# Optimization experiments

Measured on AMD Instinct MI355X. Metric: run time of the kernel, lower is better.

## Reference

```python
import jax, jax.numpy as jnp
import numpy as np

B, C, H, W = 16, 128, 48, 48
C4 = C // 4
N = H * W
BN_EPS = 1e-5


def conv_bn_relu(x, w, gamma, beta, mean, var):
    # 1x1 conv (no bias) as channel contraction, then eval-mode BatchNorm, then ReLU
    y = jnp.einsum('bchw,oc->bohw', x, w)
    scale = gamma / jnp.sqrt(var + BN_EPS)
    y = y * scale[None, :, None, None] + (beta - mean * scale)[None, :, None, None]
    return jax.nn.relu(y)


def setup_inputs() -> dict:
    key = jax.random.key(0)
    ks = jax.random.split(key, 16)
    inp = {
        'x_en': jax.random.normal(ks[0], (B, C, H, W), dtype=jnp.float32),
        'x_de': jax.random.normal(ks[1], (B, C, H, W), dtype=jnp.float32),
        'x_cat': jax.random.normal(ks[2], (B, 2 * C, H, W), dtype=jnp.float32),
        # Get_KQ: Conv2d(C -> C/4, 1x1, no bias) + BN(C/4) (shared for K and Q)
        'w_kq': jax.random.normal(ks[3], (C4, C), dtype=jnp.float32) * 0.05,
        'kq_gamma': jax.random.normal(ks[4], (C4,), dtype=jnp.float32) * 0.1 + 1.0,
        'kq_beta': jax.random.normal(ks[5], (C4,), dtype=jnp.float32) * 0.1,
        'kq_mean': jax.random.normal(ks[6], (C4,), dtype=jnp.float32) * 0.1,
        'kq_var': jax.random.uniform(ks[7], (C4,), dtype=jnp.float32) + 0.5,
        # Get_V: Conv2d(C -> C, 1x1, no bias) + BN(C)
        'w_v': jax.random.normal(ks[8], (C, C), dtype=jnp.float32) * 0.05,
        'v_gamma': jax.random.normal(ks[9], (C,), dtype=jnp.float32) * 0.1 + 1.0,
        'v_beta': jax.random.normal(ks[10], (C,), dtype=jnp.float32) * 0.1,
        'v_mean': jax.random.normal(ks[11], (C,), dtype=jnp.float32) * 0.1,
        'v_var': jax.random.uniform(ks[12], (C,), dtype=jnp.float32) + 0.5,
        # reduce_channels: Conv2d(2C -> C, 1x1, no bias) + BN(C)
        'w_red': jax.random.normal(ks[13], (C, 2 * C), dtype=jnp.float32) * 0.05,
        'red_gamma': jax.random.normal(ks[14], (C,), dtype=jnp.float32) * 0.1 + 1.0,
        'red_beta': jax.random.normal(ks[15], (C,), dtype=jnp.float32) * 0.1,
        'red_mean': jax.random.normal(jax.random.fold_in(key, 100), (C,), dtype=jnp.float32) * 0.1,
        'red_var': jax.random.uniform(jax.random.fold_in(key, 101), (C,), dtype=jnp.float32) + 0.5,
    }
    return inp


def reference(x_en, x_de, x_cat,
              w_kq, kq_gamma, kq_beta, kq_mean, kq_var,
              w_v, v_gamma, v_beta, v_mean, v_var,
              w_red, red_gamma, red_beta, red_mean, red_var):
    Kf = conv_bn_relu(x_en, w_kq, kq_gamma, kq_beta, kq_mean, kq_var).reshape(B, C4, N)
    Qf = conv_bn_relu(x_de, w_kq, kq_gamma, kq_beta, kq_mean, kq_var).reshape(B, C4, N)
    # KQ[b, n, m] = sum_k K[b, k, n] * Q[b, k, m]  -> [B, N, N]
    KQ = jnp.einsum('bkn,bkm->bnm', Kf, Qf)
    # GLOBAL softmax over the flattened N*N map (per batch), not per row
    A = jax.nn.softmax(KQ.reshape(B, N * N), axis=1).reshape(B, N, N)
    x = conv_bn_relu(x_cat, w_red, red_gamma, red_beta, red_mean, red_var)
    V = conv_bn_relu(x, w_v, v_gamma, v_beta, v_mean, v_var).reshape(B, C, N)
    # FeatureMap[b, c, n] = sum_m V[b, c, m] * A[b, n, m]
    feat = jnp.einsum('bcm,bnm->bcn', V, A).reshape(B, C, H, W)
    return jnp.concatenate([x, feat], axis=1)
```

## Files before the change

kernel.cpp:

```cpp
#include <hip/hip_runtime.h>
#include <math.h>

#define C    128
#define C4   32
#define NN   2304
#define BN_EPS 1e-5f
#define NEG_INF -3.402823466e38f
#define LOG2E 1.4426950408889634f

typedef short bf16x8 __attribute__((ext_vector_type(8)));
typedef float f32x4 __attribute__((ext_vector_type(4)));

#define SOFT_BARRIER() asm volatile("s_waitcnt lgkmcnt(0)\n\ts_barrier" ::: "memory")

__device__ inline unsigned short f2bf(float f) {
    unsigned int u = __float_as_uint(f);
    u += 0x7fffu + ((u >> 16) & 1u);
    return (unsigned short)(u >> 16);
}

__device__ inline unsigned int pk2bf(float a, float b) {
#if __has_builtin(__builtin_amdgcn_cvt_pk_bf16_f32)
    typedef __bf16 bf2 __attribute__((ext_vector_type(2)));
    bf2 v = __builtin_amdgcn_cvt_pk_bf16_f32(a, b);
    return __builtin_bit_cast(unsigned int, v);
#else
    unsigned int ua = __float_as_uint(a); ua += 0x7fffu + ((ua >> 16) & 1u);
    unsigned int ub = __float_as_uint(b); ub += 0x7fffu + ((ub >> 16) & 1u);
    return __builtin_amdgcn_perm(ub, ua, 0x07060302u);
#endif
}

__device__ inline float fexp2(float x) {
#if __has_builtin(__builtin_amdgcn_exp2f)
    return __builtin_amdgcn_exp2f(x);
#else
    return __expf(x * 0.69314718055994531f);
#endif
}


__global__ __launch_bounds__(256) void k_wprep(
    const float* __restrict__ wkq, const float* __restrict__ kq_g,
    const float* __restrict__ kq_b, const float* __restrict__ kq_m,
    const float* __restrict__ kq_v,
    const float* __restrict__ wv, const float* __restrict__ v_g,
    const float* __restrict__ v_b, const float* __restrict__ v_m,
    const float* __restrict__ v_v,
    const float* __restrict__ wred, const float* __restrict__ red_g,
    const float* __restrict__ red_b, const float* __restrict__ red_m,
    const float* __restrict__ red_v,
    unsigned short* __restrict__ wkq_bf, unsigned short* __restrict__ wv_bf,
    unsigned short* __restrict__ wred_bf,
    float* __restrict__ kq_sh, float* __restrict__ v_sh, float* __restrict__ red_sh)
{
    const int t = blockIdx.x * 256 + threadIdx.x;
    if (t < 4096) {
        const int o = t >> 7;
        const float sc = kq_g[o] * rsqrtf(kq_v[o] + BN_EPS);
        wkq_bf[t] = f2bf(wkq[t] * sc);
        if ((t & 127) == 0) kq_sh[o] = kq_b[o] - kq_m[o] * sc;
    } else if (t < 4096 + 16384) {
        const int e = t - 4096;
        const int o = e >> 7;
        const float sc = v_g[o] * rsqrtf(v_v[o] + BN_EPS);
        wv_bf[e] = f2bf(wv[e] * sc);
        if ((e & 127) == 0) v_sh[o] = v_b[o] - v_m[o] * sc;
    } else if (t < 4096 + 16384 + 32768) {
        const int e = t - 20480;
        const int o = e >> 8;
        const float sc = red_g[o] * rsqrtf(red_v[o] + BN_EPS);
        wred_bf[e] = f2bf(wred[e] * sc);
        if ((e & 255) == 0) red_sh[o] = red_b[o] - red_m[o] * sc;
    }
}

__global__ __launch_bounds__(256) void k_kq(
    const float* __restrict__ x0, const float* __restrict__ x1,
    const unsigned short* __restrict__ wbf, const float* __restrict__ shift,
    unsigned short* __restrict__ Kt, unsigned short* __restrict__ Qt)
{
    constexpr int NTILE = 128, R = 8;
    __shared__ unsigned short Xs[2][NTILE][40];

    const int tid = threadIdx.x;
    const int w = tid >> 6, lane = tid & 63;
    const int quad = lane >> 4, l16 = lane & 15;
    const int b = blockIdx.y, n0 = blockIdx.x * NTILE;
    const int nbase = w * 32;

    const float* xin = (blockIdx.z ? x1 : x0) + (size_t)b * C * NN;
    const int p = tid & 15, g = tid >> 4;

    f32x4 acc[2][2];
#pragma unroll
    for (int mt = 0; mt < 2; mt++)
#pragma unroll
        for (int nt = 0; nt < 2; nt++) acc[mt][nt] = (f32x4){0.f, 0.f, 0.f, 0.f};

    const float* xrb = xin + n0 + g * R;
    float av[R], bv[R];
    {
        const float* xr = xrb + (size_t)(2 * p) * NN;
#pragma unroll
        for (int i4 = 0; i4 < R; i4 += 4) {
            *(float4*)&av[i4] = *(const float4*)&xr[i4];
            *(float4*)&bv[i4] = *(const float4*)&xr[NN + i4];
        }
    }

    for (int k = 0; k < 4; ++k) {
        unsigned int uu[R];
#pragma unroll
        for (int i = 0; i < R; i++) uu[i] = pk2bf(av[i], bv[i]);
        if (k < 3) {
            const float* xr = xrb + (size_t)((k + 1) * 32 + 2 * p) * NN;
#pragma unroll
            for (int i4 = 0; i4 < R; i4 += 4) {
                *(float4*)&av[i4] = *(const float4*)&xr[i4];
                *(float4*)&bv[i4] = *(const float4*)&xr[NN + i4];
            }
        }
        unsigned int* Xw = (unsigned int*)Xs[k & 1];
#pragma unroll
        for (int i = 0; i < R; i++)
            Xw[(g * R + i) * 20 + p] = uu[i];
        SOFT_BARRIER();
        bf16x8 af[2];
#pragma unroll
        for (int mt = 0; mt < 2; mt++)
            af[mt] = *(const bf16x8*)&wbf[(size_t)(mt * 16 + l16) * C + k * 32 + quad * 8];
#pragma unroll
        for (int nt = 0; nt < 2; nt++) {
            const bf16x8 bfr = *(const bf16x8*)&Xs[k & 1][nbase + nt * 16 + l16][quad * 8];
#pragma unroll
            for (int mt = 0; mt < 2; mt++)
                acc[mt][nt] = __builtin_amdgcn_mfma_f32_16x16x32_bf16(af[mt], bfr, acc[mt][nt], 0, 0, 0);
        }
    }

    unsigned short* ob16 = blockIdx.z ? Qt : Kt;
    const float osc = blockIdx.z ? 1.f : LOG2E;
#pragma unroll
    for (int mt = 0; mt < 2; mt++)
#pragma unroll
        for (int nt = 0; nt < 2; nt++)
#pragma unroll
            for (int r = 0; r < 4; r++) {
                const int o = mt * 16 + quad * 4 + r;
                const int n = n0 + nbase + nt * 16 + l16;
                const float sh = shift[o];
                ob16[((size_t)b * NN + n) * 32 + o] =
                    f2bf(fmaxf(acc[mt][nt][r] + sh, 0.f) * osc);
            }
}

__global__ __launch_bounds__(256) void k_redv(
    const float* __restrict__ xcat,
    const unsigned short* __restrict__ wred_bf, const float* __restrict__ red_sh,
    const unsigned short* __restrict__ wv_bf,  const float* __restrict__ v_sh,
    float* __restrict__ out, unsigned short* __restrict__ Vf)
{
    __shared__ unsigned short Xs[2][48][40];
    __shared__ unsigned int   Xv[64 * 49];

    const int tid = threadIdx.x;
    const int w = tid >> 6, lane = tid & 63;
    const int quad = lane >> 4, l16 = lane & 15;
    const int b = blockIdx.y, n0 = blockIdx.x * 48;
    const float* xin = xcat + (size_t)b * 2 * C * NN;
    const int p = tid & 15, g = tid >> 4;

    f32x4 acc[2][3];
#pragma unroll
    for (int mt = 0; mt < 2; mt++)
#pragma unroll
        for (int nt = 0; nt < 3; nt++) acc[mt][nt] = (f32x4){0.f, 0.f, 0.f, 0.f};

    float4 av, bv;
    if (g < 12) {
        const float* xr = xin + (size_t)(2 * p) * NN + n0 + g * 4;
        av = *(const float4*)&xr[0];
        bv = *(const float4*)&xr[NN];
    }

    for (int k = 0; k < 8; ++k) {
        if (g < 12) {
            const unsigned int u0 = pk2bf(av.x, bv.x);
            const unsigned int u1 = pk2bf(av.y, bv.y);
            const unsigned int u2 = pk2bf(av.z, bv.z);
            const unsigned int u3 = pk2bf(av.w, bv.w);
            if (k < 7) {
                const float* xr = xin + (size_t)((k + 1) * 32 + 2 * p) * NN + n0 + g * 4;
                av = *(const float4*)&xr[0];
                bv = *(const float4*)&xr[NN];
            }
            unsigned int* Xw = (unsigned int*)Xs[k & 1];
            Xw[(g * 4 + 0) * 20 + p] = u0;
            Xw[(g * 4 + 1) * 20 + p] = u1;
            Xw[(g * 4 + 2) * 20 + p] = u2;
            Xw[(g * 4 + 3) * 20 + p] = u3;
        }
        SOFT_BARRIER();
        bf16x8 af[2];
#pragma unroll
        for (int mt = 0; mt < 2; mt++)
            af[mt] = *(const bf16x8*)&wred_bf[(size_t)(w * 32 + mt * 16 + l16) * (2 * C) + k * 32 + quad * 8];
#pragma unroll
        for (int nt = 0; nt < 3; nt++) {
            const bf16x8 bfr = *(const bf16x8*)&Xs[k & 1][nt * 16 + l16][quad * 8];
#pragma unroll
            for (int mt = 0; mt < 2; mt++)
                acc[mt][nt] = __builtin_amdgcn_mfma_f32_16x16x32_bf16(af[mt], bfr, acc[mt][nt], 0, 0, 0);
        }
    }

    {
        float* ob = out + (size_t)b * (2 * C * NN);
#pragma unroll
        for (int mt = 0; mt < 2; mt++) {
            float sh[4];
#pragma unroll
            for (int r = 0; r < 4; r++) sh[r] = red_sh[w * 32 + mt * 16 + quad * 4 + r];
#pragma unroll
            for (int nt = 0; nt < 3; nt++) {
                const int n = n0 + nt * 16 + l16;
                float v[4];
#pragma unroll
                for (int r = 0; r < 4; r++) {
                    const int o = w * 32 + mt * 16 + quad * 4 + r;
                    v[r] = fmaxf(acc[mt][nt][r] + sh[r], 0.f);
                    ob[(size_t)o * NN + n] = v[r];
                }
                const int op0 = 16 * w + mt * 8 + quad * 2;
                Xv[(op0 + 0) * 49 + nt * 16 + l16] = pk2bf(v[0], v[1]);
                Xv[(op0 + 1) * 49 + nt * 16 + l16] = pk2bf(v[2], v[3]);
            }
        }
    }
    SOFT_BARRIER();

    f32x4 vacc[2][3];
#pragma unroll
    for (int mt = 0; mt < 2; mt++)
#pragma unroll
        for (int nt = 0; nt < 3; nt++) vacc[mt][nt] = (f32x4){0.f, 0.f, 0.f, 0.f};

    for (int c0 = 0; c0 < C; c0 += 32) {
        bf16x8 af[2];
#pragma unroll
        for (int mt = 0; mt < 2; mt++)
            af[mt] = *(const bf16x8*)&wv_bf[(size_t)(w * 32 + mt * 16 + l16) * C + c0 + quad * 8];
#pragma unroll
        for (int nt = 0; nt < 3; nt++) {
            const int col = nt * 16 + l16;
            const int cp0 = c0 / 2 + quad * 4;
            uint4 u;
            u.x = Xv[(cp0 + 0) * 49 + col];
            u.y = Xv[(cp0 + 1) * 49 + col];
            u.z = Xv[(cp0 + 2) * 49 + col];
            u.w = Xv[(cp0 + 3) * 49 + col];
            const bf16x8 bfr = __builtin_bit_cast(bf16x8, u);
#pragma unroll
            for (int mt = 0; mt < 2; mt++)
                vacc[mt][nt] = __builtin_amdgcn_mfma_f32_16x16x32_bf16(af[mt], bfr, vacc[mt][nt], 0, 0, 0);
        }
    }

#pragma unroll
    for (int mt = 0; mt < 2; mt++) {
        float sh[4];
#pragma unroll
        for (int r = 0; r < 4; r++) sh[r] = v_sh[w * 32 + mt * 16 + quad * 4 + r];
#pragma unroll
        for (int nt = 0; nt < 3; nt++)
#pragma unroll
            for (int r = 0; r < 4; r++) {
                const int o = w * 32 + mt * 16 + quad * 4 + r;
                const int n = n0 + nt * 16 + l16;
                Vf[((size_t)b * C + o) * NN + n] = f2bf(fmaxf(vacc[mt][nt][r] + sh[r], 0.f));
            }
    }
}

__global__ __launch_bounds__(256) void k_stats(
    const unsigned short* __restrict__ Kt, const unsigned short* __restrict__ Qt,
    float* __restrict__ bmax, float* __restrict__ bsum)
{
    const int tid = threadIdx.x;
    const int w = tid >> 6, lane = tid & 63;
    const int quad = lane >> 4, l16 = lane & 15;
    const int wg = blockIdx.x;
    const int xcd = wg & 7;
    const int slot = wg >> 3;
    const int b = xcd * 2 + slot / 324;
    const int tile = slot % 324;
    const int my = tile / 18, mx = tile % 18;
    const int n0 = mx * 128, m0 = my * 128;
    const unsigned short* Kb = Kt + (size_t)b * NN * 32;
    const unsigned short* Qb = Qt + (size_t)b * NN * 32;

    bf16x8 kf[8], qf[2];
#pragma unroll
    for (int nt = 0; nt < 8; nt++)
        kf[nt] = *(const bf16x8*)&Kb[(size_t)(n0 + nt * 16 + l16) * 32 + quad * 8];
#pragma unroll
    for (int mt = 0; mt < 2; mt++)
        qf[mt] = *(const bf16x8*)&Qb[(size_t)(m0 + w * 32 + mt * 16 + l16) * 32 + quad * 8];

    f32x4 s[16];
#pragma unroll
    for (int mt = 0; mt < 2; mt++)
#pragma unroll
        for (int nt = 0; nt < 8; nt++) {
            f32x4 z = (f32x4){0.f, 0.f, 0.f, 0.f};
            s[mt * 8 + nt] = __builtin_amdgcn_mfma_f32_16x16x32_bf16(qf[mt], kf[nt], z, 0, 0, 0);
        }

    float lmax = NEG_INF;
#pragma unroll
    for (int i = 0; i < 16; i++)
        lmax = fmaxf(lmax, fmaxf(fmaxf(s[i][0], s[i][1]), fmaxf(s[i][2], s[i][3])));
    float lsum = 0.f;
#pragma unroll
    for (int i = 0; i < 16; i++)
        lsum += fexp2(s[i][0] - lmax) + fexp2(s[i][1] - lmax) +
                fexp2(s[i][2] - lmax) + fexp2(s[i][3] - lmax);

#pragma unroll
    for (int off = 32; off > 0; off >>= 1) {
        const float omax = __shfl_xor(lmax, off);
        const float osum = __shfl_xor(lsum, off);
        const float nmax = fmaxf(lmax, omax);
        lsum = lsum * fexp2(lmax - nmax) + osum * fexp2(omax - nmax);
        lmax = nmax;
    }
    __shared__ float smax[4], ssum[4];
    if (lane == 0) { smax[w] = lmax; ssum[w] = lsum; }
    __syncthreads();
    if (tid == 0) {
        float M = smax[0], S = ssum[0];
        for (int i = 1; i < 4; i++) {
            const float nmax = fmaxf(M, smax[i]);
            S = S * fexp2(M - nmax) + ssum[i] * fexp2(smax[i] - nmax);
            M = nmax;
        }
        const int idx = (b * 18 + my) * 18 + mx;
        bmax[idx] = M;
        bsum[idx] = S;
    }
}

__global__ __launch_bounds__(256) void k_fin(
    const float* __restrict__ bmax, const float* __restrict__ bsum,
    float* __restrict__ Ms, float* __restrict__ Sinv)
{
    __shared__ float rmax[256], rsum[256];
    const int b = blockIdx.x, tid = threadIdx.x;
    float lmax = NEG_INF, lsum = 0.f;
    for (int i = tid; i < 324; i += 256) {
        const float m = bmax[b * 324 + i], s = bsum[b * 324 + i];
        const float nmax = fmaxf(lmax, m);
        lsum = lsum * fexp2(lmax - nmax) + s * fexp2(m - nmax);
        lmax = nmax;
    }
    rmax[tid] = lmax; rsum[tid] = lsum;
    __syncthreads();
    for (int st = 128; st > 0; st >>= 1) {
        if (tid < st) {
            const float m2 = rmax[tid + st], s2 = rsum[tid + st];
            const float nmax = fmaxf(rmax[tid], m2);
            rsum[tid] = rsum[tid] * fexp2(rmax[tid] - nmax) + s2 * fexp2(m2 - nmax);
            rmax[tid] = nmax;
        }
        __syncthreads();
    }
    if (tid == 0) { Ms[b] = rmax[0]; Sinv[b] = 1.f / rsum[0]; }
}

__global__ __launch_bounds__(256) void k_feat(
    const unsigned short* __restrict__ Kt, const unsigned short* __restrict__ Qt,
    const unsigned short* __restrict__ Vf, const float* __restrict__ Ms,
    const float* __restrict__ Sinv, float* __restrict__ out)
{
    __shared__ __align__(16) unsigned short Et[2][48][136];
    const int tid = threadIdx.x;
    const int w = tid >> 6, lane = tid & 63;
    const int quad = lane >> 4, l16 = lane & 15;
    const int wg = blockIdx.x;
    const int xcd = wg & 7;
    const int slot = wg >> 3;
    const int b = xcd * 2 + slot / 48;
    const int n0 = (slot % 48) * 48;
    const unsigned short* Kb = Kt + (size_t)b * NN * 32;
    const unsigned short* Qb = Qt + (size_t)b * NN * 32;
    const unsigned short* Vb = Vf + (size_t)b * C * NN;
    const float M = Ms[b], Si = Sinv[b];

    bf16x8 kf[3];
#pragma unroll
    for (int nt = 0; nt < 3; nt++)
        kf[nt] = *(const bf16x8*)&Kb[(size_t)(n0 + nt * 16 + l16) * 32 + quad * 8];

    f32x4 acc[2][3];
#pragma unroll
    for (int i = 0; i < 2; i++)
#pragma unroll
        for (int j = 0; j < 3; j++) acc[i][j] = (f32x4){0.f, 0.f, 0.f, 0.f};

    {
        const bf16x8 q00 = *(const bf16x8*)&Qb[(size_t)(w * 32 + l16) * 32 + quad * 8];
        const bf16x8 q01 = *(const bf16x8*)&Qb[(size_t)(w * 32 + 16 + l16) * 32 + quad * 8];
        f32x4 s0[3], s1[3];
#pragma unroll
        for (int nt = 0; nt < 3; nt++) {
            f32x4 z = (f32x4){0.f, 0.f, 0.f, 0.f};
            s0[nt] = __builtin_amdgcn_mfma_f32_16x16x32_bf16(q00, kf[nt], z, 0, 0, 0);
            s1[nt] = __builtin_amdgcn_mfma_f32_16x16x32_bf16(q01, kf[nt], z, 0, 0, 0);
        }
#pragma unroll
        for (int nt = 0; nt < 3; nt++) {
            const unsigned int a0 = pk2bf(fexp2(s0[nt][0] - M), fexp2(s0[nt][1] - M));
            const unsigned int a1 = pk2bf(fexp2(s0[nt][2] - M), fexp2(s0[nt][3] - M));
            *(uint2*)&Et[0][nt * 16 + l16][w * 32 + quad * 4] = make_uint2(a0, a1);
            const unsigned int b0 = pk2bf(fexp2(s1[nt][0] - M), fexp2(s1[nt][1] - M));
            const unsigned int b1 = pk2bf(fexp2(s1[nt][2] - M), fexp2(s1[nt][3] - M));
            *(uint2*)&Et[0][nt * 16 + l16][w * 32 + 16 + quad * 4] = make_uint2(b0, b1);
        }
    }
    bf16x8 qc0 = *(const bf16x8*)&Qb[(size_t)(128 + w * 32 + l16) * 32 + quad * 8];
    bf16x8 qc1 = *(const bf16x8*)&Qb[(size_t)(128 + w * 32 + 16 + l16) * 32 + quad * 8];
    SOFT_BARRIER();

    for (int k = 0; k < 18; ++k) {
        const int cur = k & 1;
        const int m0 = k * 128;
        const int mq = (k + 2 < 18 ? k + 2 : 0) * 128;
        bf16x8 qn0 = *(const bf16x8*)&Qb[(size_t)(mq + w * 32 + l16) * 32 + quad * 8];
        bf16x8 qn1 = *(const bf16x8*)&Qb[(size_t)(mq + w * 32 + 16 + l16) * 32 + quad * 8];
        bf16x8 vc[2][4];
#pragma unroll
        for (int ct = 0; ct < 2; ct++)
#pragma unroll
            for (int ks = 0; ks < 4; ks++)
                vc[ct][ks] = *(const bf16x8*)&Vb[(size_t)(w * 32 + ct * 16 + l16) * NN + m0 + ks * 32 + quad * 8];

        if (k < 17) {
            f32x4 s0[3], s1[3];
#pragma unroll
            for (int nt = 0; nt < 3; nt++) {
                f32x4 z = (f32x4){0.f, 0.f, 0.f, 0.f};
                s0[nt] = __builtin_amdgcn_mfma_f32_16x16x32_bf16(qc0, kf[nt], z, 0, 0, 0);
                s1[nt] = __builtin_amdgcn_mfma_f32_16x16x32_bf16(qc1, kf[nt], z, 0, 0, 0);
            }
#pragma unroll
            for (int nt = 0; nt < 3; nt++) {
                const unsigned int a0 = pk2bf(fexp2(s0[nt][0] - M), fexp2(s0[nt][1] - M));
                const unsigned int a1 = pk2bf(fexp2(s0[nt][2] - M), fexp2(s0[nt][3] - M));
                *(uint2*)&Et[cur ^ 1][nt * 16 + l16][w * 32 + quad * 4] = make_uint2(a0, a1);
                const unsigned int b0 = pk2bf(fexp2(s1[nt][0] - M), fexp2(s1[nt][1] - M));
                const unsigned int b1 = pk2bf(fexp2(s1[nt][2] - M), fexp2(s1[nt][3] - M));
                *(uint2*)&Et[cur ^ 1][nt * 16 + l16][w * 32 + 16 + quad * 4] = make_uint2(b0, b1);
            }
        }

        __builtin_amdgcn_s_setprio(1);
#pragma unroll
        for (int ks = 0; ks < 4; ks++) {
#pragma unroll
            for (int nt = 0; nt < 3; nt++) {
                const bf16x8 ef = *(const bf16x8*)&Et[cur][nt * 16 + l16][ks * 32 + quad * 8];
                acc[0][nt] = __builtin_amdgcn_mfma_f32_16x16x32_bf16(vc[0][ks], ef, acc[0][nt], 0, 0, 0);
                acc[1][nt] = __builtin_amdgcn_mfma_f32_16x16x32_bf16(vc[1][ks], ef, acc[1][nt], 0, 0, 0);
            }
        }
        __builtin_amdgcn_s_setprio(0);
        SOFT_BARRIER();
        qc0 = qn0;
        qc1 = qn1;
    }

    float* ob = out + (size_t)b * 2 * C * NN + (size_t)C * NN + n0;
#pragma unroll
    for (int ct = 0; ct < 2; ct++)
#pragma unroll
        for (int nt = 0; nt < 3; nt++)
#pragma unroll
            for (int r = 0; r < 4; r++) {
                const int c = w * 32 + ct * 16 + quad * 4 + r;
                ob[(size_t)c * NN + nt * 16 + l16] = acc[ct][nt][r] * Si;
            }
}

extern "C" void kernel_launch(void* const* d_in, const int* in_sizes, int n_in,
                              void* d_out, int out_size, void* d_ws, size_t ws_size,
                              hipStream_t stream)
{
    const float* x_en   = (const float*)d_in[0];
    const float* x_de   = (const float*)d_in[1];
    const float* x_cat  = (const float*)d_in[2];
    const float* w_kq   = (const float*)d_in[3];
    const float* kq_g   = (const float*)d_in[4];
    const float* kq_b   = (const float*)d_in[5];
    const float* kq_m   = (const float*)d_in[6];
    const float* kq_v   = (const float*)d_in[7];
    const float* w_v    = (const float*)d_in[8];
    const float* v_g    = (const float*)d_in[9];
    const float* v_b    = (const float*)d_in[10];
    const float* v_m    = (const float*)d_in[11];
    const float* v_v    = (const float*)d_in[12];
    const float* w_red  = (const float*)d_in[13];
    const float* red_g  = (const float*)d_in[14];
    const float* red_b  = (const float*)d_in[15];
    const float* red_m  = (const float*)d_in[16];
    const float* red_v  = (const float*)d_in[17];

    unsigned short* Kt      = (unsigned short*)d_ws;
    unsigned short* Qt      = Kt + 1179648;
    unsigned short* Vf      = Qt + 1179648;
    unsigned short* wkq_bf  = Vf + 4718592;
    unsigned short* wv_bf   = wkq_bf + 4096;
    unsigned short* wred_bf = wv_bf + 16384;
    float* bmax = (float*)(wred_bf + 32768);
    float* bsum = bmax + 16 * 324;
    float* Ms   = bsum + 16 * 324;
    float* Sinv = Ms + 16;
    float* kq_sh  = Sinv + 16;
    float* v_sh   = kq_sh + 32;
    float* red_sh = v_sh + 128;
    float* out  = (float*)d_out;

    k_wprep<<<208, 256, 0, stream>>>(
        w_kq, kq_g, kq_b, kq_m, kq_v,
        w_v, v_g, v_b, v_m, v_v,
        w_red, red_g, red_b, red_m, red_v,
        wkq_bf, wv_bf, wred_bf, kq_sh, v_sh, red_sh);

    k_kq  <<<dim3(18, 16, 2), 256, 0, stream>>>(x_en, x_de, wkq_bf, kq_sh, Kt, Qt);
    k_redv<<<dim3(48, 16), 256, 0, stream>>>(x_cat, wred_bf, red_sh, wv_bf, v_sh, out, Vf);

    k_stats<<<5184, 256, 0, stream>>>(Kt, Qt, bmax, bsum);
    k_fin  <<<16, 256, 0, stream>>>(bmax, bsum, Ms, Sinv);
    k_feat <<<768, 256, 0, stream>>>(Kt, Qt, Vf, Ms, Sinv, out);
}
```

Baseline: 249.2 us.

## Merge KQ and red/V projection kernels and tile V layout for feat loads

The separate K/Q projection kernel and reduce+V kernel become one launch of 1344 blocks, with a shared raw shared-memory buffer and branching on the block index. This removes one launch and lets the two independent workloads run at the same time. V is also stored in a tiled [b][n/32][c][32] bf16 layout, so each k_feat step reads contiguous 32-element chunks per channel row instead of rows strided by NN. The combined kernel uses the larger shared-memory footprint for every block, which may reduce occupancy for the KQ blocks.

```diff
diff --git a/kernel.cpp b/kernel.cpp
--- a/kernel.cpp
+++ b/kernel.cpp
@@ -75,211 +75,215 @@
     }
 }
 
-__global__ __launch_bounds__(256) void k_kq(
+__global__ __launch_bounds__(256) void k_kqredv(
     const float* __restrict__ x0, const float* __restrict__ x1,
+    const float* __restrict__ xcat,
     const unsigned short* __restrict__ wbf, const float* __restrict__ shift,
-    unsigned short* __restrict__ Kt, unsigned short* __restrict__ Qt)
-{
-    constexpr int NTILE = 128, R = 8;
-    __shared__ unsigned short Xs[2][NTILE][40];
-
-    const int tid = threadIdx.x;
-    const int w = tid >> 6, lane = tid & 63;
-    const int quad = lane >> 4, l16 = lane & 15;
-    const int b = blockIdx.y, n0 = blockIdx.x * NTILE;
-    const int nbase = w * 32;
-
-    const float* xin = (blockIdx.z ? x1 : x0) + (size_t)b * C * NN;
-    const int p = tid & 15, g = tid >> 4;
-
-    f32x4 acc[2][2];
-#pragma unroll
-    for (int mt = 0; mt < 2; mt++)
-#pragma unroll
-        for (int nt = 0; nt < 2; nt++) acc[mt][nt] = (f32x4){0.f, 0.f, 0.f, 0.f};
-
-    const float* xrb = xin + n0 + g * R;
-    float av[R], bv[R];
-    {
-        const float* xr = xrb + (size_t)(2 * p) * NN;
-#pragma unroll
-        for (int i4 = 0; i4 < R; i4 += 4) {
-            *(float4*)&av[i4] = *(const float4*)&xr[i4];
-            *(float4*)&bv[i4] = *(const float4*)&xr[NN + i4];
-        }
-    }
-
-    for (int k = 0; k < 4; ++k) {
-        unsigned int uu[R];
-#pragma unroll
-        for (int i = 0; i < R; i++) uu[i] = pk2bf(av[i], bv[i]);
-        if (k < 3) {
-            const float* xr = xrb + (size_t)((k + 1) * 32 + 2 * p) * NN;
-#pragma unroll
-            for (int i4 = 0; i4 < R; i4 += 4) {
-                *(float4*)&av[i4] = *(const float4*)&xr[i4];
-                *(float4*)&bv[i4] = *(const float4*)&xr[NN + i4];
-            }
-        }
-        unsigned int* Xw = (unsigned int*)Xs[k & 1];
-#pragma unroll
-        for (int i = 0; i < R; i++)
-            Xw[(g * R + i) * 20 + p] = uu[i];
-        SOFT_BARRIER();
-        bf16x8 af[2];
-#pragma unroll
-        for (int mt = 0; mt < 2; mt++)
-            af[mt] = *(const bf16x8*)&wbf[(size_t)(mt * 16 + l16) * C + k * 32 + quad * 8];
-#pragma unroll
-        for (int nt = 0; nt < 2; nt++) {
-            const bf16x8 bfr = *(const bf16x8*)&Xs[k & 1][nbase + nt * 16 + l16][quad * 8];
-#pragma unroll
-            for (int mt = 0; mt < 2; mt++)
-                acc[mt][nt] = __builtin_amdgcn_mfma_f32_16x16x32_bf16(af[mt], bfr, acc[mt][nt], 0, 0, 0);
-        }
-    }
-
-    unsigned short* ob16 = blockIdx.z ? Qt : Kt;
-    const float osc = blockIdx.z ? 1.f : LOG2E;
-#pragma unroll
-    for (int mt = 0; mt < 2; mt++)
-#pragma unroll
-        for (int nt = 0; nt < 2; nt++)
-#pragma unroll
-            for (int r = 0; r < 4; r++) {
-                const int o = mt * 16 + quad * 4 + r;
-                const int n = n0 + nbase + nt * 16 + l16;
-                const float sh = shift[o];
-                ob16[((size_t)b * NN + n) * 32 + o] =
-                    f2bf(fmaxf(acc[mt][nt][r] + sh, 0.f) * osc);
-            }
-}
-
-__global__ __launch_bounds__(256) void k_redv(
-    const float* __restrict__ xcat,
+    unsigned short* __restrict__ Kt, unsigned short* __restrict__ Qt,
     const unsigned short* __restrict__ wred_bf, const float* __restrict__ red_sh,
     const unsigned short* __restrict__ wv_bf,  const float* __restrict__ v_sh,
     float* __restrict__ out, unsigned short* __restrict__ Vf)
 {
-    __shared__ unsigned short Xs[2][48][40];
-    __shared__ unsigned int   Xv[64 * 49];
-
+    __shared__ __align__(16) unsigned char smem[20608];
+    const int wg = blockIdx.x;
     const int tid = threadIdx.x;
     const int w = tid >> 6, lane = tid & 63;
     const int quad = lane >> 4, l16 = lane & 15;
-    const int b = blockIdx.y, n0 = blockIdx.x * 48;
-    const float* xin = xcat + (size_t)b * 2 * C * NN;
     const int p = tid & 15, g = tid >> 4;
 
-    f32x4 acc[2][3];
-#pragma unroll
-    for (int mt = 0; mt < 2; mt++)
-#pragma unroll
-        for (int nt = 0; nt < 3; nt++) acc[mt][nt] = (f32x4){0.f, 0.f, 0.f, 0.f};
-
-    float4 av, bv;
-    if (g < 12) {
-        const float* xr = xin + (size_t)(2 * p) * NN + n0 + g * 4;
-        av = *(const float4*)&xr[0];
-        bv = *(const float4*)&xr[NN];
-    }
-
-    for (int k = 0; k < 8; ++k) {
+    if (wg < 768) {
+        typedef unsigned short XsT[48][40];
+        XsT* Xs = (XsT*)smem;
+        unsigned int* Xv = (unsigned int*)(smem + 7680);
+
+        const int b = wg / 48, n0 = (wg % 48) * 48;
+        const float* xin = xcat + (size_t)b * 2 * C * NN;
+
+        f32x4 acc[2][3];
+#pragma unroll
+        for (int mt = 0; mt < 2; mt++)
+#pragma unroll
+            for (int nt = 0; nt < 3; nt++) acc[mt][nt] = (f32x4){0.f, 0.f, 0.f, 0.f};
+
+        float4 av, bv;
         if (g < 12) {
-            const unsigned int u0 = pk2bf(av.x, bv.x);
-            const unsigned int u1 = pk2bf(av.y, bv.y);
-            const unsigned int u2 = pk2bf(av.z, bv.z);
-            const unsigned int u3 = pk2bf(av.w, bv.w);
-            if (k < 7) {
-                const float* xr = xin + (size_t)((k + 1) * 32 + 2 * p) * NN + n0 + g * 4;
-                av = *(const float4*)&xr[0];
-                bv = *(const float4*)&xr[NN];
-            }
-            unsigned int* Xw = (unsigned int*)Xs[k & 1];
-            Xw[(g * 4 + 0) * 20 + p] = u0;
-            Xw[(g * 4 + 1) * 20 + p] = u1;
-            Xw[(g * 4 + 2) * 20 + p] = u2;
-            Xw[(g * 4 + 3) * 20 + p] = u3;
+            const float* xr = xin + (size_t)(2 * p) * NN + n0 + g * 4;
+            av = *(const float4*)&xr[0];
+            bv = *(const float4*)&xr[NN];
+        }
+
+        for (int k = 0; k < 8; ++k) {
+            if (g < 12) {
+                const unsigned int u0 = pk2bf(av.x, bv.x);
+                const unsigned int u1 = pk2bf(av.y, bv.y);
+                const unsigned int u2 = pk2bf(av.z, bv.z);
+                const unsigned int u3 = pk2bf(av.w, bv.w);
+                if (k < 7) {
+                    const float* xr = xin + (size_t)((k + 1) * 32 + 2 * p) * NN + n0 + g * 4;
+                    av = *(const float4*)&xr[0];
+                    bv = *(const float4*)&xr[NN];
+                }
+                unsigned int* Xw = (unsigned int*)Xs[k & 1];
+                Xw[(g * 4 + 0) * 20 + p] = u0;
+                Xw[(g * 4 + 1) * 20 + p] = u1;
+                Xw[(g * 4 + 2) * 20 + p] = u2;
+                Xw[(g * 4 + 3) * 20 + p] = u3;
+            }
+            SOFT_BARRIER();
+            bf16x8 af[2];
+#pragma unroll
+            for (int mt = 0; mt < 2; mt++)
+                af[mt] = *(const bf16x8*)&wred_bf[(size_t)(w * 32 + mt * 16 + l16) * (2 * C) + k * 32 + quad * 8];
+#pragma unroll
+            for (int nt = 0; nt < 3; nt++) {
+                const bf16x8 bfr = *(const bf16x8*)&Xs[k & 1][nt * 16 + l16][quad * 8];
+#pragma unroll
+                for (int mt = 0; mt < 2; mt++)
+                    acc[mt][nt] = __builtin_amdgcn_mfma_f32_16x16x32_bf16(af[mt], bfr, acc[mt][nt], 0, 0, 0);
+            }
+        }
+
+        {
+            float* ob = out + (size_t)b * (2 * C * NN);
+#pragma unroll
+            for (int mt = 0; mt < 2; mt++) {
+                float sh[4];
+#pragma unroll
+                for (int r = 0; r < 4; r++) sh[r] = red_sh[w * 32 + mt * 16 + quad * 4 + r];
+#pragma unroll
+                for (int nt = 0; nt < 3; nt++) {
+                    const int n = n0 + nt * 16 + l16;
+                    float v[4];
+#pragma unroll
+                    for (int r = 0; r < 4; r++) {
+                        const int o = w * 32 + mt * 16 + quad * 4 + r;
+                        v[r] = fmaxf(acc[mt][nt][r] + sh[r], 0.f);
+                        ob[(size_t)o * NN + n] = v[r];
+                    }
+                    const int op0 = 16 * w + mt * 8 + quad * 2;
+                    Xv[(op0 + 0) * 49 + nt * 16 + l16] = pk2bf(v[0], v[1]);
+                    Xv[(op0 + 1) * 49 + nt * 16 + l16] = pk2bf(v[2], v[3]);
+                }
+            }
         }
         SOFT_BARRIER();
-        bf16x8 af[2];
+
+        f32x4 vacc[2][3];
 #pragma unroll
         for (int mt = 0; mt < 2; mt++)
-            af[mt] = *(const bf16x8*)&wred_bf[(size_t)(w * 32 + mt * 16 + l16) * (2 * C) + k * 32 + quad * 8];
-#pragma unroll
-        for (int nt = 0; nt < 3; nt++) {
-            const bf16x8 bfr = *(const bf16x8*)&Xs[k & 1][nt * 16 + l16][quad * 8];
+#pragma unroll
+            for (int nt = 0; nt < 3; nt++) vacc[mt][nt] = (f32x4){0.f, 0.f, 0.f, 0.f};
+
+        for (int c0 = 0; c0 < C; c0 += 32) {
+            bf16x8 af[2];
 #pragma unroll
             for (int mt = 0; mt < 2; mt++)
-                acc[mt][nt] = __builtin_amdgcn_mfma_f32_16x16x32_bf16(af[mt], bfr, acc[mt][nt], 0, 0, 0);
-        }
-    }
-
-    {
-        float* ob = out + (size_t)b * (2 * C * NN);
+                af[mt] = *(const bf16x8*)&wv_bf[(size_t)(w * 32 + mt * 16 + l16) * C + c0 + quad * 8];
+#pragma unroll
+            for (int nt = 0; nt < 3; nt++) {
+                const int col = nt * 16 + l16;
+                const int cp0 = c0 / 2 + quad * 4;
+                uint4 u;
+                u.x = Xv[(cp0 + 0) * 49 + col];
+                u.y = Xv[(cp0 + 1) * 49 + col];
+                u.z = Xv[(cp0 + 2) * 49 + col];
+                u.w = Xv[(cp0 + 3) * 49 + col];
+                const bf16x8 bfr = __builtin_bit_cast(bf16x8, u);
+#pragma unroll
+                for (int mt = 0; mt < 2; mt++)
+                    vacc[mt][nt] = __builtin_amdgcn_mfma_f32_16x16x32_bf16(af[mt], bfr, vacc[mt][nt], 0, 0, 0);
+            }
+        }
+
 #pragma unroll
         for (int mt = 0; mt < 2; mt++) {
             float sh[4];
 #pragma unroll
-            for (int r = 0; r < 4; r++) sh[r] = red_sh[w * 32 + mt * 16 + quad * 4 + r];
-#pragma unroll
-            for (int nt = 0; nt < 3; nt++) {
-                const int n = n0 + nt * 16 + l16;
-                float v[4];
+            for (int r = 0; r < 4; r++) sh[r] = v_sh[w * 32 + mt * 16 + quad * 4 + r];
+#pragma unroll
+            for (int nt = 0; nt < 3; nt++)
 #pragma unroll
                 for (int r = 0; r < 4; r++) {
                     const int o = w * 32 + mt * 16 + quad * 4 + r;
-                    v[r] = fmaxf(acc[mt][nt][r] + sh[r], 0.f);
-                    ob[(size_t)o * NN + n] = v[r];
+                    const int n = n0 + nt * 16 + l16;
+                    Vf[(((size_t)b * 72 + (n >> 5)) * 128 + o) * 32 + (n & 31)] =
+                        f2bf(fmaxf(vacc[mt][nt][r] + sh[r], 0.f));
                 }
-                const int op0 = 16 * w + mt * 8 + quad * 2;
-                Xv[(op0 + 0) * 49 + nt * 16 + l16] = pk2bf(v[0], v[1]);
-                Xv[(op0 + 1) * 49 + nt * 16 + l16] = pk2bf(v[2], v[3]);
-            }
-        }
-    }
-    SOFT_BARRIER();
-
-    f32x4 vacc[2][3];
-#pragma unroll
-    for (int mt = 0; mt < 2; mt++)
-#pragma unroll
-        for (int nt = 0; nt < 3; nt++) vacc[mt][nt] = (f32x4){0.f, 0.f, 0.f, 0.f};
-
-    for (int c0 = 0; c0 < C; c0 += 32) {
-        bf16x8 af[2];
+        }
+    } else {
+        typedef unsigned short Xs2T[128][40];
+        Xs2T* Xs = (Xs2T*)smem;
+        constexpr int R = 8;
+
+        const int e = wg - 768;
+        const int z = e / 288;
+        const int rem = e - z * 288;
+        const int b = rem / 18, n0 = (rem % 18) * 128;
+        const int nbase = w * 32;
+
+        const float* xin = (z ? x1 : x0) + (size_t)b * C * NN;
+
+        f32x4 acc[2][2];
 #pragma unroll
         for (int mt = 0; mt < 2; mt++)
-            af[mt] = *(const bf16x8*)&wv_bf[(size_t)(w * 32 + mt * 16 + l16) * C + c0 + quad * 8];
-#pragma unroll
-        for (int nt = 0; nt < 3; nt++) {
-            const int col = nt * 16 + l16;
-            const int cp0 = c0 / 2 + quad * 4;
-            uint4 u;
-            u.x = Xv[(cp0 + 0) * 49 + col];
-            u.y = Xv[(cp0 + 1) * 49 + col];
-            u.z = Xv[(cp0 + 2) * 49 + col];
-            u.w = Xv[(cp0 + 3) * 49 + col];
-            const bf16x8 bfr = __builtin_bit_cast(bf16x8, u);
+#pragma unroll
+            for (int nt = 0; nt < 2; nt++) acc[mt][nt] = (f32x4){0.f, 0.f, 0.f, 0.f};
+
+        const float* xrb = xin + n0 + g * R;
+        float av[R], bv[R];
+        {
+            const float* xr = xrb + (size_t)(2 * p) * NN;
+#pragma unroll
+            for (int i4 = 0; i4 < R; i4 += 4) {
+                *(float4*)&av[i4] = *(const float4*)&xr[i4];
+                *(float4*)&bv[i4] = *(const float4*)&xr[NN + i4];
+            }
+        }
+
+        for (int k = 0; k < 4; ++k) {
+            unsigned int uu[R];
+#pragma unroll
+            for (int i = 0; i < R; i++) uu[i] = pk2bf(av[i], bv[i]);
+            if (k < 3) {
+                const float* xr = xrb + (size_t)((k + 1) * 32 + 2 * p) * NN;
+#pragma unroll
+                for (int i4 = 0; i4 < R; i4 += 4) {
+                    *(float4*)&av[i4] = *(const float4*)&xr[i4];
+                    *(float4*)&bv[i4] = *(const float4*)&xr[NN + i4];
+                }
+            }
+            unsigned int* Xw = (unsigned int*)Xs[k & 1];
+#pragma unroll
+            for (int i = 0; i < R; i++)
+                Xw[(g * R + i) * 20 + p] = uu[i];
+            SOFT_BARRIER();
+            bf16x8 af[2];
 #pragma unroll
             for (int mt = 0; mt < 2; mt++)
-                vacc[mt][nt] = __builtin_amdgcn_mfma_f32_16x16x32_bf16(af[mt], bfr, vacc[mt][nt], 0, 0, 0);
-        }
-    }
-
-#pragma unroll
-    for (int mt = 0; mt < 2; mt++) {
-        float sh[4];
-#pragma unroll
-        for (int r = 0; r < 4; r++) sh[r] = v_sh[w * 32 + mt * 16 + quad * 4 + r];
-#pragma unroll
-        for (int nt = 0; nt < 3; nt++)
-#pragma unroll
-            for (int r = 0; r < 4; r++) {
-                const int o = w * 32 + mt * 16 + quad * 4 + r;
-                const int n = n0 + nt * 16 + l16;
-                Vf[((size_t)b * C + o) * NN + n] = f2bf(fmaxf(vacc[mt][nt][r] + sh[r], 0.f));
-            }
+                af[mt] = *(const bf16x8*)&wbf[(size_t)(mt * 16 + l16) * C + k * 32 + quad * 8];
+#pragma unroll
+            for (int nt = 0; nt < 2; nt++) {
+                const bf16x8 bfr = *(const bf16x8*)&Xs[k & 1][nbase + nt * 16 + l16][quad * 8];
+#pragma unroll
+                for (int mt = 0; mt < 2; mt++)
+                    acc[mt][nt] = __builtin_amdgcn_mfma_f32_16x16x32_bf16(af[mt], bfr, acc[mt][nt], 0, 0, 0);
+            }
+        }
+
+        unsigned short* ob16 = z ? Qt : Kt;
+        const float osc = z ? 1.f : LOG2E;
+#pragma unroll
+        for (int mt = 0; mt < 2; mt++)
+#pragma unroll
+            for (int nt = 0; nt < 2; nt++)
+#pragma unroll
+                for (int r = 0; r < 4; r++) {
+                    const int o = mt * 16 + quad * 4 + r;
+                    const int n = n0 + nbase + nt * 16 + l16;
+                    const float sh = shift[o];
+                    ob16[((size_t)b * NN + n) * 32 + o] =
+                        f2bf(fmaxf(acc[mt][nt][r] + sh, 0.f) * osc);
+                }
     }
 }
 
@@ -394,7 +398,7 @@
     const int n0 = (slot % 48) * 48;
     const unsigned short* Kb = Kt + (size_t)b * NN * 32;
     const unsigned short* Qb = Qt + (size_t)b * NN * 32;
-    const unsigned short* Vb = Vf + (size_t)b * C * NN;
+    const unsigned short* Vb = Vf + (size_t)b * 72 * 128 * 32;
     const float M = Ms[b], Si = Sinv[b];
 
     bf16x8 kf[3];
@@ -434,7 +438,7 @@
 
     for (int k = 0; k < 18; ++k) {
         const int cur = k & 1;
-        const int m0 = k * 128;
+        const int mt0 = k * 4;
         const int mq = (k + 2 < 18 ? k + 2 : 0) * 128;
         bf16x8 qn0 = *(const bf16x8*)&Qb[(size_t)(mq + w * 32 + l16) * 32 + quad * 8];
         bf16x8 qn1 = *(const bf16x8*)&Qb[(size_t)(mq + w * 32 + 16 + l16) * 32 + quad * 8];
@@ -443,7 +447,7 @@
         for (int ct = 0; ct < 2; ct++)
 #pragma unroll
             for (int ks = 0; ks < 4; ks++)
-                vc[ct][ks] = *(const bf16x8*)&Vb[(size_t)(w * 32 + ct * 16 + l16) * NN + m0 + ks * 32 + quad * 8];
+                vc[ct][ks] = *(const bf16x8*)&Vb[(((size_t)(mt0 + ks)) * 128 + w * 32 + ct * 16 + l16) * 32 + quad * 8];
 
         if (k < 17) {
             f32x4 s0[3], s1[3];
@@ -536,8 +540,9 @@
         w_red, red_g, red_b, red_m, red_v,
         wkq_bf, wv_bf, wred_bf, kq_sh, v_sh, red_sh);
 
-    k_kq  <<<dim3(18, 16, 2), 256, 0, stream>>>(x_en, x_de, wkq_bf, kq_sh, Kt, Qt);
-    k_redv<<<dim3(48, 16), 256, 0, stream>>>(x_cat, wred_bf, red_sh, wv_bf, v_sh, out, Vf);
+    k_kqredv<<<1344, 256, 0, stream>>>(
+        x_en, x_de, x_cat, wkq_bf, kq_sh, Kt, Qt,
+        wred_bf, red_sh, wv_bf, v_sh, out, Vf);
 
     k_stats<<<5184, 256, 0, stream>>>(Kt, Qt, bmax, bsum);
     k_fin  <<<16, 256, 0, stream>>>(bmax, bsum, Ms, Sinv);
```

Measured after the change: 224.7 us. 1.11x faster.
